# Kernel tuning notes

Hardware: AMD Instinct MI355X
Metric: run time of the kernel (lower is better)

Reference implementation:

```python
import jax, jax.numpy as jnp
import numpy as np

# OmniNet(deepqmc) reconstruction: ElectronicSchNet v1 (2 interactions, kernel_dim=8,
# embedding_dim=16, dist_feat_dim=4) + Linear(16,1,bias=False) orbital + sum over electrons.
# SchNet v1: shared w and g per interaction, spin-dependent h (same/anti), nuclear
# messages via learned nuclear embeddings Y. Subnets: w = 2-layer log-DNN 4->6->8 with SSP,
# h = Linear(16,8), g = Linear(8,16). SSP(x) = softplus(x) - log(2).

N_UP, N_DOWN = 16, 16
N_ELEC = N_UP + N_DOWN
N_ATOMS = 8
DIST_FEAT, KERNEL, EMBED = 4, 8, 16
N_INTER = 2
BATCH = 4096


def ssp(x):
    return jax.nn.softplus(x) - jnp.log(2.0).astype(x.dtype)


def setup_inputs() -> dict:
    key = jax.random.key(0)
    ks = jax.random.split(key, 16)
    s = 0.5  # init scale
    return {
        'dists_nuc': jax.random.uniform(ks[0], (BATCH, N_ELEC, N_ATOMS, DIST_FEAT), jnp.float32),
        'dists_elec': jax.random.uniform(ks[1], (BATCH, N_ELEC, N_ELEC, DIST_FEAT), jnp.float32),
        'X': jax.random.normal(ks[2], (1, EMBED), jnp.float32) * s,          # electron embedding (n_up==n_down)
        'Y': jax.random.normal(ks[3], (N_ATOMS, KERNEL), jnp.float32) * s,   # nuclear embeddings
        'w1': jax.random.normal(ks[4], (N_INTER, DIST_FEAT, 6), jnp.float32) * s,
        'wb1': jax.random.normal(ks[5], (N_INTER, 6), jnp.float32) * s,
        'w2': jax.random.normal(ks[6], (N_INTER, 6, KERNEL), jnp.float32) * s,
        'wb2': jax.random.normal(ks[7], (N_INTER, KERNEL), jnp.float32) * s,
        'hs_w': jax.random.normal(ks[8], (N_INTER, EMBED, KERNEL), jnp.float32) * s,
        'hs_b': jax.random.normal(ks[9], (N_INTER, KERNEL), jnp.float32) * s,
        'ha_w': jax.random.normal(ks[10], (N_INTER, EMBED, KERNEL), jnp.float32) * s,
        'ha_b': jax.random.normal(ks[11], (N_INTER, KERNEL), jnp.float32) * s,
        'g_w': jax.random.normal(ks[12], (N_INTER, KERNEL, EMBED), jnp.float32) * s,
        'g_b': jax.random.normal(ks[13], (N_INTER, EMBED), jnp.float32) * s,
        'orb_w': jax.random.normal(ks[14], (EMBED,), jnp.float32) * s,
    }


def reference(dists_nuc, dists_elec, X, Y, w1, wb1, w2, wb2, hs_w, hs_b, ha_w, ha_b, g_w, g_b, orb_w):
    B, n_elec = dists_elec.shape[:2]
    dt = dists_elec.dtype
    spins = jnp.concatenate([jnp.zeros(N_UP, jnp.int32), jnp.ones(N_DOWN, jnp.int32)])
    eye = jnp.eye(n_elec, dtype=bool)
    same = ((spins[:, None] == spins[None, :]) & ~eye).astype(dt)  # (i,j) same-spin, no self
    anti = (spins[:, None] != spins[None, :]).astype(dt)

    # initial embeddings: all electrons share X[0] since n_up == n_down
    x = jnp.broadcast_to(X[0], (B, n_elec, EMBED))

    for n in range(N_INTER):
        def w_net(e):  # (..., 4) -> (..., 8)
            return ssp(e @ w1[n] + wb1[n]) @ w2[n] + wb2[n]
        we = w_net(dists_elec)            # (B, i, j, K)
        wn = w_net(dists_nuc)             # (B, i, M, K)
        hs = x @ hs_w[n] + hs_b[n]        # (B, j, K) same-spin message features
        ha = x @ ha_w[n] + ha_b[n]        # (B, j, K) anti-spin
        z = (jnp.einsum('bijk,ij,bjk->bik', we, same, hs)
             + jnp.einsum('bijk,ij,bjk->bik', we, anti, ha)
             + jnp.einsum('bimk,mk->bik', wn, Y))
        x = x + (z @ g_w[n] + g_b[n])     # residual update

    # orbital projection (Linear(16,1,bias=False)), squeeze, sum over electrons
    return (x @ orb_w).sum(axis=-1)       # (B,)
```

## Files before the change

### kernel.cpp

```cpp
#include <hip/hip_runtime.h>

#define NE 32
#define NA 8
#define DF 4
#define KD 8
#define ED 16
#define BATCH 4096

__device__ __forceinline__ float sspf(float v) {
    float sp = fmaxf(v, 0.0f) + __logf(1.0f + __expf(-fabsf(v)));
    return sp - 0.69314718055994531f;
}

__global__ __launch_bounds__(256) void omni_kernel(
    const float* __restrict__ dists_nuc,
    const float* __restrict__ dists_elec,
    const float* __restrict__ X,
    const float* __restrict__ Y,
    const float* __restrict__ w1,
    const float* __restrict__ wb1,
    const float* __restrict__ w2,
    const float* __restrict__ wb2,
    const float* __restrict__ hs_w,
    const float* __restrict__ hs_b,
    const float* __restrict__ ha_w,
    const float* __restrict__ ha_b,
    const float* __restrict__ g_w,
    const float* __restrict__ g_b,
    const float* __restrict__ orb_w,
    float* __restrict__ out)
{
    const int tid  = threadIdx.x;
    const int wv   = tid >> 6;
    const int lane = tid & 63;
    const int i    = lane & 31;
    const int h    = lane >> 5;
    const int b    = blockIdx.x * 4 + wv;

    __shared__ float msg[4][2][NE][KD];

    float x[ED];
    #pragma unroll
    for (int c = 0; c < ED; ++c) x[c] = X[c];

    const float* de = dists_elec + (((size_t)b * NE + i) * NE) * DF;
    const float* dn = dists_nuc  + (((size_t)b * NE + i) * NA) * DF;

    const int si = i >> 4;

    #pragma unroll 1
    for (int n = 0; n < 2; ++n) {
        float W1[DF][6], B1[6], W2[6][KD], B2[KD];
        {
            const float* p1  = w1  + n * DF * 6;
            const float* pb1 = wb1 + n * 6;
            const float* p2  = w2  + n * 6 * KD;
            const float* pb2 = wb2 + n * KD;
            #pragma unroll
            for (int d = 0; d < DF; ++d)
                #pragma unroll
                for (int a = 0; a < 6; ++a) W1[d][a] = p1[d * 6 + a];
            #pragma unroll
            for (int a = 0; a < 6; ++a) B1[a] = pb1[a];
            #pragma unroll
            for (int a = 0; a < 6; ++a)
                #pragma unroll
                for (int k = 0; k < KD; ++k) W2[a][k] = p2[a * KD + k];
            #pragma unroll
            for (int k = 0; k < KD; ++k) B2[k] = pb2[k];
        }

        {
            const float* mw = (h == 0 ? hs_w : ha_w) + n * ED * KD;
            const float* mb = (h == 0 ? hs_b : ha_b) + n * KD;
            float mi[KD];
            #pragma unroll
            for (int k = 0; k < KD; ++k) mi[k] = mb[k];
            #pragma unroll
            for (int c = 0; c < ED; ++c) {
                const float xc = x[c];
                #pragma unroll
                for (int k = 0; k < KD; ++k) mi[k] = fmaf(xc, mw[c * KD + k], mi[k]);
            }
            __syncthreads();
            #pragma unroll
            for (int k = 0; k < KD; ++k) msg[wv][h][i][k] = mi[k];
            __syncthreads();
        }

        float z[KD];
        #pragma unroll
        for (int k = 0; k < KD; ++k) z[k] = 0.0f;

        const int t = (h == si) ? 0 : 1;
        const float* mrow = &msg[wv][t][0][0];
        #pragma unroll 4
        for (int s = 0; s < 16; ++s) {
            const int j = 16 * h + s;
            const float4 e = *(const float4*)(de + j * DF);
            float act[6];
            #pragma unroll
            for (int a = 0; a < 6; ++a)
                act[a] = sspf(fmaf(e.x, W1[0][a], fmaf(e.y, W1[1][a],
                              fmaf(e.z, W1[2][a], fmaf(e.w, W1[3][a], B1[a])))));
            const float mask = (j == i) ? 0.0f : 1.0f;
            #pragma unroll
            for (int k = 0; k < KD; ++k) {
                float wvk = B2[k];
                #pragma unroll
                for (int a = 0; a < 6; ++a) wvk = fmaf(act[a], W2[a][k], wvk);
                z[k] = fmaf(wvk, mrow[j * KD + k] * mask, z[k]);
            }
        }

        #pragma unroll
        for (int s = 0; s < 4; ++s) {
            const int m = 4 * h + s;
            const float4 e = *(const float4*)(dn + m * DF);
            float act[6];
            #pragma unroll
            for (int a = 0; a < 6; ++a)
                act[a] = sspf(fmaf(e.x, W1[0][a], fmaf(e.y, W1[1][a],
                              fmaf(e.z, W1[2][a], fmaf(e.w, W1[3][a], B1[a])))));
            #pragma unroll
            for (int k = 0; k < KD; ++k) {
                float wvk = B2[k];
                #pragma unroll
                for (int a = 0; a < 6; ++a) wvk = fmaf(act[a], W2[a][k], wvk);
                z[k] = fmaf(wvk, Y[m * KD + k], z[k]);
            }
        }

        #pragma unroll
        for (int k = 0; k < KD; ++k) z[k] += __shfl_xor(z[k], 32, 64);

        #pragma unroll
        for (int c = 0; c < ED; ++c) {
            float acc = g_b[n * ED + c];
            #pragma unroll
            for (int k = 0; k < KD; ++k)
                acc = fmaf(z[k], g_w[n * KD * ED + k * ED + c], acc);
            x[c] += acc;
        }
    }

    float dot = 0.0f;
    #pragma unroll
    for (int c = 0; c < ED; ++c) dot = fmaf(x[c], orb_w[c], dot);
    dot *= 0.5f;
    #pragma unroll
    for (int off = 32; off > 0; off >>= 1) dot += __shfl_xor(dot, off, 64);
    if (lane == 0) out[b] = dot;
}

extern "C" void kernel_launch(void* const* d_in, const int* in_sizes, int n_in,
                              void* d_out, int out_size, void* d_ws, size_t ws_size,
                              hipStream_t stream) {
    const float* dists_nuc  = (const float*)d_in[0];
    const float* dists_elec = (const float*)d_in[1];
    const float* X     = (const float*)d_in[2];
    const float* Y     = (const float*)d_in[3];
    const float* w1    = (const float*)d_in[4];
    const float* wb1   = (const float*)d_in[5];
    const float* w2    = (const float*)d_in[6];
    const float* wb2   = (const float*)d_in[7];
    const float* hs_w  = (const float*)d_in[8];
    const float* hs_b  = (const float*)d_in[9];
    const float* ha_w  = (const float*)d_in[10];
    const float* ha_b  = (const float*)d_in[11];
    const float* g_w   = (const float*)d_in[12];
    const float* g_b   = (const float*)d_in[13];
    const float* orb_w = (const float*)d_in[14];
    float* out = (float*)d_out;

    dim3 grid(BATCH / 4), block(256);
    omni_kernel<<<grid, block, 0, stream>>>(dists_nuc, dists_elec, X, Y,
                                            w1, wb1, w2, wb2,
                                            hs_w, hs_b, ha_w, ha_b,
                                            g_w, g_b, orb_w, out);
}
```

Baseline: 177.9 us.

## Split each batch element across two wavefronts and pack SSP w-net math in float2

Each batch element is now handled by two wavefronts, so four lanes share the j and nucleus loops and the grid doubles. Partial z sums are combined through a shared-memory buffer. The SSP subnet now computes two samples at once with packed float2 FMAs and raw exp2/log builtins. The log(2) shift and the ln scaling are folded algebraically into the biases and one final multiply. Self-pair masking reads a zero row in LDS instead of a multiply. In exchange it adds an extra block barrier, more blocks, and drops the numerically stable softplus form, so large inputs can overflow exp2.

```diff
diff --git a/kernel.cpp b/kernel.cpp
--- a/kernel.cpp
+++ b/kernel.cpp
@@ -7,9 +7,55 @@
 #define ED 16
 #define BATCH 4096
 
-__device__ __forceinline__ float sspf(float v) {
-    float sp = fmaxf(v, 0.0f) + __logf(1.0f + __expf(-fabsf(v)));
-    return sp - 0.69314718055994531f;
+typedef float f32x2 __attribute__((ext_vector_type(2)));
+
+__device__ __forceinline__ f32x2 splat2(float s) { f32x2 r; r.x = s; r.y = s; return r; }
+__device__ __forceinline__ f32x2 fma2(f32x2 a, f32x2 b, f32x2 c) {
+    return __builtin_elementwise_fma(a, b, c);
+}
+
+__device__ __forceinline__ void wnet2(const float4 e0, const float4 e1,
+                                      const f32x2* __restrict__ B1s,
+                                      const float* __restrict__ pW1,
+                                      const float* __restrict__ pW2,
+                                      const f32x2* __restrict__ B2h,
+                                      f32x2* __restrict__ wv)
+{
+    const float LOG2E = 1.4426950408889634f;
+    f32x2 ex, ey, ez, ew;
+    ex.x = e0.x; ex.y = e1.x;
+    ey.x = e0.y; ey.y = e1.y;
+    ez.x = e0.z; ez.y = e1.z;
+    ew.x = e0.w; ew.y = e1.w;
+    ex = ex * splat2(LOG2E);
+    ey = ey * splat2(LOG2E);
+    ez = ez * splat2(LOG2E);
+    ew = ew * splat2(LOG2E);
+
+    f32x2 r[6];
+    #pragma unroll
+    for (int a = 0; a < 6; ++a) {
+        f32x2 u = B1s[a];
+        u = fma2(ex, splat2(pW1[0 * 6 + a]), u);
+        u = fma2(ey, splat2(pW1[1 * 6 + a]), u);
+        u = fma2(ez, splat2(pW1[2 * 6 + a]), u);
+        u = fma2(ew, splat2(pW1[3 * 6 + a]), u);
+        f32x2 t;
+        t.x = __builtin_amdgcn_exp2f(u.x);
+        t.y = __builtin_amdgcn_exp2f(u.y);
+        t = t + splat2(1.0f);
+        r[a].x = __builtin_amdgcn_logf(t.x);
+        r[a].y = __builtin_amdgcn_logf(t.y);
+    }
+
+    #pragma unroll
+    for (int k = 0; k < KD; ++k) {
+        f32x2 acc = B2h[k];
+        #pragma unroll
+        for (int a = 0; a < 6; ++a)
+            acc = fma2(r[a], splat2(pW2[a * KD + k]), acc);
+        wv[k] = acc;
+    }
 }
 
 __global__ __launch_bounds__(256) void omni_kernel(
@@ -31,48 +77,55 @@
     float* __restrict__ out)
 {
     const int tid  = threadIdx.x;
-    const int wv   = tid >> 6;
+    const int wid  = tid >> 6;
+    const int el   = wid >> 1;
+    const int q    = wid & 1;
     const int lane = tid & 63;
     const int i    = lane & 31;
-    const int h    = lane >> 5;
-    const int b    = blockIdx.x * 4 + wv;
-
-    __shared__ float msg[4][2][NE][KD];
+    const int p    = lane >> 5;
+    const int qq   = 2 * q + p;
+    const int b    = blockIdx.x * 2 + el;
+    const int si   = i >> 4;
+    const int t32  = (q == si) ? 0 : 32;
+
+    __shared__ float msg[2][65][KD];
+    __shared__ float zbuf[2][2][NE][KD];
+
+    if (q == 0 && lane < KD) msg[el][64][lane] = 0.0f;
 
     float x[ED];
     #pragma unroll
     for (int c = 0; c < ED; ++c) x[c] = X[c];
 
-    const float* de = dists_elec + (((size_t)b * NE + i) * NE) * DF;
-    const float* dn = dists_nuc  + (((size_t)b * NE + i) * NA) * DF;
-
-    const int si = i >> 4;
+    const float* de = dists_elec + ((size_t)b * NE + i) * NE * DF;
+    const float* dn = dists_nuc  + ((size_t)b * NE + i) * NA * DF;
+
+    const float LOG2E = 1.4426950408889634f;
+    const float LN2   = 0.6931471805599453f;
 
     #pragma unroll 1
     for (int n = 0; n < 2; ++n) {
-        float W1[DF][6], B1[6], W2[6][KD], B2[KD];
+        const float* pW1 = w1  + n * DF * 6;
+        const float* pB1 = wb1 + n * 6;
+        const float* pW2 = w2  + n * 6 * KD;
+        const float* pB2 = wb2 + n * KD;
+
+        f32x2 B1s[6];
+        #pragma unroll
+        for (int a = 0; a < 6; ++a) B1s[a] = splat2(pB1[a] * LOG2E);
+
+        f32x2 B2h[KD];
+        #pragma unroll
+        for (int k = 0; k < KD; ++k) {
+            float sw = pW2[0 * KD + k];
+            #pragma unroll
+            for (int a = 1; a < 6; ++a) sw += pW2[a * KD + k];
+            B2h[k] = splat2(fmaf(pB2[k], LOG2E, -sw));
+        }
+
         {
-            const float* p1  = w1  + n * DF * 6;
-            const float* pb1 = wb1 + n * 6;
-            const float* p2  = w2  + n * 6 * KD;
-            const float* pb2 = wb2 + n * KD;
-            #pragma unroll
-            for (int d = 0; d < DF; ++d)
-                #pragma unroll
-                for (int a = 0; a < 6; ++a) W1[d][a] = p1[d * 6 + a];
-            #pragma unroll
-            for (int a = 0; a < 6; ++a) B1[a] = pb1[a];
-            #pragma unroll
-            for (int a = 0; a < 6; ++a)
-                #pragma unroll
-                for (int k = 0; k < KD; ++k) W2[a][k] = p2[a * KD + k];
-            #pragma unroll
-            for (int k = 0; k < KD; ++k) B2[k] = pb2[k];
-        }
-
-        {
-            const float* mw = (h == 0 ? hs_w : ha_w) + n * ED * KD;
-            const float* mb = (h == 0 ? hs_b : ha_b) + n * KD;
+            const float* mw = (q == 0 ? hs_w : ha_w) + n * ED * KD;
+            const float* mb = (q == 0 ? hs_b : ha_b) + n * KD;
             float mi[KD];
             #pragma unroll
             for (int k = 0; k < KD; ++k) mi[k] = mb[k];
@@ -83,56 +136,63 @@
                 for (int k = 0; k < KD; ++k) mi[k] = fmaf(xc, mw[c * KD + k], mi[k]);
             }
             __syncthreads();
-            #pragma unroll
-            for (int k = 0; k < KD; ++k) msg[wv][h][i][k] = mi[k];
+            if (p == 0) {
+                #pragma unroll
+                for (int k = 0; k < KD; ++k) msg[el][q * 32 + i][k] = mi[k];
+            }
             __syncthreads();
         }
 
+        float zl[KD], zh[KD];
+        #pragma unroll
+        for (int k = 0; k < KD; ++k) { zl[k] = 0.0f; zh[k] = 0.0f; }
+
+        #pragma unroll
+        for (int s = 0; s < 4; ++s) {
+            const int j0 = 8 * qq + 2 * s;
+            const int j1 = j0 + 1;
+            const float4 e0 = *(const float4*)(de + j0 * DF);
+            const float4 e1 = *(const float4*)(de + j1 * DF);
+            f32x2 wv[KD];
+            wnet2(e0, e1, B1s, pW1, pW2, B2h, wv);
+            const float* m0 = &msg[el][(j0 == i) ? 64 : (t32 + j0)][0];
+            const float* m1 = &msg[el][(j1 == i) ? 64 : (t32 + j1)][0];
+            #pragma unroll
+            for (int k = 0; k < KD; ++k) {
+                zl[k] = fmaf(wv[k].x, m0[k], zl[k]);
+                zh[k] = fmaf(wv[k].y, m1[k], zh[k]);
+            }
+        }
+
+        {
+            const int m0i = 2 * qq;
+            const int m1i = m0i + 1;
+            const float4 f0 = *(const float4*)(dn + m0i * DF);
+            const float4 f1 = *(const float4*)(dn + m1i * DF);
+            f32x2 wv[KD];
+            wnet2(f0, f1, B1s, pW1, pW2, B2h, wv);
+            const float* y0 = Y + m0i * KD;
+            const float* y1 = Y + m1i * KD;
+            #pragma unroll
+            for (int k = 0; k < KD; ++k) {
+                zl[k] = fmaf(wv[k].x, y0[k], zl[k]);
+                zh[k] = fmaf(wv[k].y, y1[k], zh[k]);
+            }
+        }
+
         float z[KD];
         #pragma unroll
-        for (int k = 0; k < KD; ++k) z[k] = 0.0f;
-
-        const int t = (h == si) ? 0 : 1;
-        const float* mrow = &msg[wv][t][0][0];
-        #pragma unroll 4
-        for (int s = 0; s < 16; ++s) {
-            const int j = 16 * h + s;
-            const float4 e = *(const float4*)(de + j * DF);
-            float act[6];
-            #pragma unroll
-            for (int a = 0; a < 6; ++a)
-                act[a] = sspf(fmaf(e.x, W1[0][a], fmaf(e.y, W1[1][a],
-                              fmaf(e.z, W1[2][a], fmaf(e.w, W1[3][a], B1[a])))));
-            const float mask = (j == i) ? 0.0f : 1.0f;
-            #pragma unroll
-            for (int k = 0; k < KD; ++k) {
-                float wvk = B2[k];
-                #pragma unroll
-                for (int a = 0; a < 6; ++a) wvk = fmaf(act[a], W2[a][k], wvk);
-                z[k] = fmaf(wvk, mrow[j * KD + k] * mask, z[k]);
-            }
-        }
-
-        #pragma unroll
-        for (int s = 0; s < 4; ++s) {
-            const int m = 4 * h + s;
-            const float4 e = *(const float4*)(dn + m * DF);
-            float act[6];
-            #pragma unroll
-            for (int a = 0; a < 6; ++a)
-                act[a] = sspf(fmaf(e.x, W1[0][a], fmaf(e.y, W1[1][a],
-                              fmaf(e.z, W1[2][a], fmaf(e.w, W1[3][a], B1[a])))));
-            #pragma unroll
-            for (int k = 0; k < KD; ++k) {
-                float wvk = B2[k];
-                #pragma unroll
-                for (int a = 0; a < 6; ++a) wvk = fmaf(act[a], W2[a][k], wvk);
-                z[k] = fmaf(wvk, Y[m * KD + k], z[k]);
-            }
-        }
-
+        for (int k = 0; k < KD; ++k) z[k] = (zl[k] + zh[k]) * LN2;
         #pragma unroll
         for (int k = 0; k < KD; ++k) z[k] += __shfl_xor(z[k], 32, 64);
+
+        if (p == 0) {
+            #pragma unroll
+            for (int k = 0; k < KD; ++k) zbuf[el][q][i][k] = z[k];
+        }
+        __syncthreads();
+        #pragma unroll
+        for (int k = 0; k < KD; ++k) z[k] += zbuf[el][1 - q][i][k];
 
         #pragma unroll
         for (int c = 0; c < ED; ++c) {
@@ -150,7 +210,7 @@
     dot *= 0.5f;
     #pragma unroll
     for (int off = 32; off > 0; off >>= 1) dot += __shfl_xor(dot, off, 64);
-    if (lane == 0) out[b] = dot;
+    if (q == 0 && lane == 0) out[b] = dot;
 }
 
 extern "C" void kernel_launch(void* const* d_in, const int* in_sizes, int n_in,
@@ -173,7 +233,7 @@
     const float* orb_w = (const float*)d_in[14];
     float* out = (float*)d_out;
 
-    dim3 grid(BATCH / 4), block(256);
+    dim3 grid(BATCH / 2), block(256);
     omni_kernel<<<grid, block, 0, stream>>>(dists_nuc, dists_elec, X, Y,
                                             w1, wb1, w2, wb2,
                                             hs_w, hs_b, ha_w, ha_b,
```

After: 192.6 us. 1.08x slower.

## Restructure SSP in base-2 with folded constants and remap threads per batch

Applied to the files above, without the earlier changes.

Rewrites the softplus-minus-log2 activation as log2(1+exp2(u)), with LOG2E folded into the first-layer inputs and bias. The constant offsets are folded into a precomputed second-layer bias, and a single LN2 scale is applied after the reduction, which removes per-element max/abs/subtract work. The thread mapping changes to one 128-thread block per batch element, with 4 lanes splitting the j range per electron. The self-pair mask is replaced by a zero row in shared memory. Dropping the max(v,0) split risks overflow of exp2 for large pre-activations, and the extra shuffle reductions add some cost.

```diff
diff --git a/kernel.cpp b/kernel.cpp
--- a/kernel.cpp
+++ b/kernel.cpp
@@ -7,12 +7,39 @@
 #define ED 16
 #define BATCH 4096
 
-__device__ __forceinline__ float sspf(float v) {
-    float sp = fmaxf(v, 0.0f) + __logf(1.0f + __expf(-fabsf(v)));
-    return sp - 0.69314718055994531f;
+__device__ __forceinline__ float exp2_fast(float v) { return __builtin_amdgcn_exp2f(v); }
+__device__ __forceinline__ float log2_fast(float v) { return __builtin_amdgcn_logf(v); }
+
+__device__ __forceinline__ void wnet1(const float4 e,
+                                      const float* __restrict__ B1s,
+                                      const float* __restrict__ pW1,
+                                      const float* __restrict__ pW2,
+                                      const float* __restrict__ B2h,
+                                      float* __restrict__ racc)
+{
+    const float LOG2E = 1.4426950408889634f;
+    const float ex = e.x * LOG2E, ey = e.y * LOG2E;
+    const float ez = e.z * LOG2E, ew = e.w * LOG2E;
+    float r[6];
+    #pragma unroll
+    for (int a = 0; a < 6; ++a) {
+        float u = B1s[a];
+        u = fmaf(ex, pW1[0 * 6 + a], u);
+        u = fmaf(ey, pW1[1 * 6 + a], u);
+        u = fmaf(ez, pW1[2 * 6 + a], u);
+        u = fmaf(ew, pW1[3 * 6 + a], u);
+        r[a] = log2_fast(exp2_fast(u) + 1.0f);
+    }
+    #pragma unroll
+    for (int k = 0; k < KD; ++k) {
+        float acc = B2h[k];
+        #pragma unroll
+        for (int a = 0; a < 6; ++a) acc = fmaf(r[a], pW2[a * KD + k], acc);
+        racc[k] = acc;
+    }
 }
 
-__global__ __launch_bounds__(256) void omni_kernel(
+__global__ __launch_bounds__(128, 4) void omni_kernel(
     const float* __restrict__ dists_nuc,
     const float* __restrict__ dists_elec,
     const float* __restrict__ X,
@@ -31,108 +58,120 @@
     float* __restrict__ out)
 {
     const int tid  = threadIdx.x;
-    const int wv   = tid >> 6;
+    const int h    = tid >> 6;
     const int lane = tid & 63;
-    const int i    = lane & 31;
-    const int h    = lane >> 5;
-    const int b    = blockIdx.x * 4 + wv;
-
-    __shared__ float msg[4][2][NE][KD];
+    const int il   = lane & 15;
+    const int jh   = lane >> 4;
+    const int ig   = 16 * h + il;
+    const int b    = blockIdx.x;
+    const int sj   = jh >> 1;
+    const int t32  = (sj == h) ? 0 : 32;
+
+    __shared__ float msg[2][65][KD];
+    __shared__ float part[2];
+
+    if (tid < 16) msg[tid >> 3][64][tid & 7] = 0.0f;
 
     float x[ED];
     #pragma unroll
     for (int c = 0; c < ED; ++c) x[c] = X[c];
 
-    const float* de = dists_elec + (((size_t)b * NE + i) * NE) * DF;
-    const float* dn = dists_nuc  + (((size_t)b * NE + i) * NA) * DF;
-
-    const int si = i >> 4;
+    const float* de = dists_elec + (((size_t)b * NE + ig) * NE + 8 * jh) * DF;
+    const float* dn = dists_nuc  + (((size_t)b * NE + ig) * NA + 2 * jh) * DF;
+
+    const float LOG2E = 1.4426950408889634f;
+    const float LN2   = 0.6931471805599453f;
 
     #pragma unroll 1
     for (int n = 0; n < 2; ++n) {
-        float W1[DF][6], B1[6], W2[6][KD], B2[KD];
+        const float* pW1 = w1  + n * DF * 6;
+        const float* pB1 = wb1 + n * 6;
+        const float* pW2 = w2  + n * 6 * KD;
+        const float* pB2 = wb2 + n * KD;
+
+        float B1s[6];
+        #pragma unroll
+        for (int a = 0; a < 6; ++a) B1s[a] = pB1[a] * LOG2E;
+
+        float B2h[KD];
+        #pragma unroll
+        for (int k = 0; k < KD; ++k) {
+            float sw = pW2[k];
+            #pragma unroll
+            for (int a = 1; a < 6; ++a) sw += pW2[a * KD + k];
+            B2h[k] = fmaf(pB2[k], LOG2E, -sw);
+        }
+
         {
-            const float* p1  = w1  + n * DF * 6;
-            const float* pb1 = wb1 + n * 6;
-            const float* p2  = w2  + n * 6 * KD;
-            const float* pb2 = wb2 + n * KD;
-            #pragma unroll
-            for (int d = 0; d < DF; ++d)
-                #pragma unroll
-                for (int a = 0; a < 6; ++a) W1[d][a] = p1[d * 6 + a];
-            #pragma unroll
-            for (int a = 0; a < 6; ++a) B1[a] = pb1[a];
-            #pragma unroll
-            for (int a = 0; a < 6; ++a)
-                #pragma unroll
-                for (int k = 0; k < KD; ++k) W2[a][k] = p2[a * KD + k];
-            #pragma unroll
-            for (int k = 0; k < KD; ++k) B2[k] = pb2[k];
-        }
-
-        {
-            const float* mw = (h == 0 ? hs_w : ha_w) + n * ED * KD;
-            const float* mb = (h == 0 ? hs_b : ha_b) + n * KD;
-            float mi[KD];
-            #pragma unroll
-            for (int k = 0; k < KD; ++k) mi[k] = mb[k];
+            float ms[KD], ma[KD];
+            #pragma unroll
+            for (int k = 0; k < KD; ++k) { ms[k] = hs_b[n * KD + k]; ma[k] = ha_b[n * KD + k]; }
             #pragma unroll
             for (int c = 0; c < ED; ++c) {
                 const float xc = x[c];
                 #pragma unroll
-                for (int k = 0; k < KD; ++k) mi[k] = fmaf(xc, mw[c * KD + k], mi[k]);
+                for (int k = 0; k < KD; ++k) {
+                    ms[k] = fmaf(xc, hs_w[n * ED * KD + c * KD + k], ms[k]);
+                    ma[k] = fmaf(xc, ha_w[n * ED * KD + c * KD + k], ma[k]);
+                }
+            }
+            if (jh == 0) {
+                #pragma unroll
+                for (int k = 0; k < KD; ++k) msg[n][ig][k] = ms[k];
+            } else if (jh == 2) {
+                #pragma unroll
+                for (int k = 0; k < KD; ++k) msg[n][32 + ig][k] = ma[k];
             }
             __syncthreads();
-            #pragma unroll
-            for (int k = 0; k < KD; ++k) msg[wv][h][i][k] = mi[k];
-            __syncthreads();
         }
 
         float z[KD];
         #pragma unroll
         for (int k = 0; k < KD; ++k) z[k] = 0.0f;
 
-        const int t = (h == si) ? 0 : 1;
-        const float* mrow = &msg[wv][t][0][0];
-        #pragma unroll 4
-        for (int s = 0; s < 16; ++s) {
-            const int j = 16 * h + s;
-            const float4 e = *(const float4*)(de + j * DF);
-            float act[6];
-            #pragma unroll
-            for (int a = 0; a < 6; ++a)
-                act[a] = sspf(fmaf(e.x, W1[0][a], fmaf(e.y, W1[1][a],
-                              fmaf(e.z, W1[2][a], fmaf(e.w, W1[3][a], B1[a])))));
-            const float mask = (j == i) ? 0.0f : 1.0f;
-            #pragma unroll
-            for (int k = 0; k < KD; ++k) {
-                float wvk = B2[k];
-                #pragma unroll
-                for (int a = 0; a < 6; ++a) wvk = fmaf(act[a], W2[a][k], wvk);
-                z[k] = fmaf(wvk, mrow[j * KD + k] * mask, z[k]);
-            }
-        }
-
-        #pragma unroll
-        for (int s = 0; s < 4; ++s) {
-            const int m = 4 * h + s;
-            const float4 e = *(const float4*)(dn + m * DF);
-            float act[6];
-            #pragma unroll
-            for (int a = 0; a < 6; ++a)
-                act[a] = sspf(fmaf(e.x, W1[0][a], fmaf(e.y, W1[1][a],
-                              fmaf(e.z, W1[2][a], fmaf(e.w, W1[3][a], B1[a])))));
-            #pragma unroll
-            for (int k = 0; k < KD; ++k) {
-                float wvk = B2[k];
-                #pragma unroll
-                for (int a = 0; a < 6; ++a) wvk = fmaf(act[a], W2[a][k], wvk);
-                z[k] = fmaf(wvk, Y[m * KD + k], z[k]);
-            }
-        }
-
-        #pragma unroll
-        for (int k = 0; k < KD; ++k) z[k] += __shfl_xor(z[k], 32, 64);
+        #pragma unroll
+        for (int s = 0; s < 8; ++s) {
+            const int j = 8 * jh + s;
+            const float4 e = ((const float4*)de)[s];
+            float racc[KD];
+            wnet1(e, B1s, pW1, pW2, B2h, racc);
+            const int row = (j == ig) ? 64 : (t32 + j);
+            const float4 m0 = *(const float4*)&msg[n][row][0];
+            const float4 m1 = *(const float4*)&msg[n][row][4];
+            z[0] = fmaf(racc[0], m0.x, z[0]);
+            z[1] = fmaf(racc[1], m0.y, z[1]);
+            z[2] = fmaf(racc[2], m0.z, z[2]);
+            z[3] = fmaf(racc[3], m0.w, z[3]);
+            z[4] = fmaf(racc[4], m1.x, z[4]);
+            z[5] = fmaf(racc[5], m1.y, z[5]);
+            z[6] = fmaf(racc[6], m1.z, z[6]);
+            z[7] = fmaf(racc[7], m1.w, z[7]);
+        }
+
+        #pragma unroll
+        for (int t = 0; t < 2; ++t) {
+            const int m = 2 * jh + t;
+            const float4 e = ((const float4*)dn)[t];
+            float racc[KD];
+            wnet1(e, B1s, pW1, pW2, B2h, racc);
+            const float4 y0 = ((const float4*)Y)[m * 2];
+            const float4 y1 = ((const float4*)Y)[m * 2 + 1];
+            z[0] = fmaf(racc[0], y0.x, z[0]);
+            z[1] = fmaf(racc[1], y0.y, z[1]);
+            z[2] = fmaf(racc[2], y0.z, z[2]);
+            z[3] = fmaf(racc[3], y0.w, z[3]);
+            z[4] = fmaf(racc[4], y1.x, z[4]);
+            z[5] = fmaf(racc[5], y1.y, z[5]);
+            z[6] = fmaf(racc[6], y1.z, z[6]);
+            z[7] = fmaf(racc[7], y1.w, z[7]);
+        }
+
+        #pragma unroll
+        for (int k = 0; k < KD; ++k) {
+            z[k] += __shfl_xor(z[k], 16, 64);
+            z[k] += __shfl_xor(z[k], 32, 64);
+            z[k] *= LN2;
+        }
 
         #pragma unroll
         for (int c = 0; c < ED; ++c) {
@@ -147,10 +186,12 @@
     float dot = 0.0f;
     #pragma unroll
     for (int c = 0; c < ED; ++c) dot = fmaf(x[c], orb_w[c], dot);
-    dot *= 0.5f;
-    #pragma unroll
-    for (int off = 32; off > 0; off >>= 1) dot += __shfl_xor(dot, off, 64);
-    if (lane == 0) out[b] = dot;
+    dot *= 0.25f;
+    #pragma unroll
+    for (int off = 1; off < 64; off <<= 1) dot += __shfl_xor(dot, off, 64);
+    if (lane == 0) part[h] = dot;
+    __syncthreads();
+    if (tid == 0) out[b] = part[0] + part[1];
 }
 
 extern "C" void kernel_launch(void* const* d_in, const int* in_sizes, int n_in,
@@ -173,7 +214,7 @@
     const float* orb_w = (const float*)d_in[14];
     float* out = (float*)d_out;
 
-    dim3 grid(BATCH / 4), block(256);
+    dim3 grid(BATCH), block(128);
     omni_kernel<<<grid, block, 0, stream>>>(dists_nuc, dists_elec, X, Y,
                                             w1, wb1, w2, wb2,
                                             hs_w, hs_b, ha_w, ha_b,
```

Result: faster. 167.7 us (-5.7%).
